# Kernel tuning notes

Measured on AMD Instinct MI355X. Metric: run time of the kernel, lower is better.

## Reference

```python
import jax, jax.numpy as jnp
import numpy as np

N, E = 20000, 160000
D_IN, HID, HEADS = 256, 64, 10
NEG_SLOPE = 0.2


def setup_inputs() -> dict:
    key = jax.random.key(0)
    ks = jax.random.split(key, 12)
    s = 0.05
    f = jnp.float32
    return {
        "x": jax.random.normal(ks[0], (N, D_IN), f),
        "edge_index": jax.random.randint(ks[1], (2, E), 0, N, jnp.int32),
        # GATConv 1: in=D_IN, out=HID, heads=10, concat=True
        "W1": (jax.random.normal(ks[2], (D_IN, HEADS * HID), f) * s),
        "a_src1": (jax.random.normal(ks[3], (HEADS, HID), f) * s),
        "a_dst1": (jax.random.normal(ks[4], (HEADS, HID), f) * s),
        "b1": jnp.zeros((HEADS * HID,), f),
        # GATConv 2: in=HEADS*HID, out=HID, heads=1
        "W2": (jax.random.normal(ks[5], (HEADS * HID, HID), f) * s),
        "a_src2": (jax.random.normal(ks[6], (1, HID), f) * s),
        "a_dst2": (jax.random.normal(ks[7], (1, HID), f) * s),
        "b2": jnp.zeros((HID,), f),
        # final Linear(hidden_dim, hidden_dim)
        "Wfc": (jax.random.normal(ks[8], (HID, HID), f) * s),
        "bfc": jnp.zeros((HID,), f),
    }


def gat_conv(x, src, dst, n, W, a_src, a_dst, b, heads, concat):
    """PyG GATConv (eval mode): gather, leaky-relu scores, segment softmax, scatter."""
    c = W.shape[1] // heads
    h = (x @ W).reshape(n, heads, c)                      # [N, H, C]
    score_src = jnp.sum(h * a_src, axis=-1)               # [N, H]
    score_dst = jnp.sum(h * a_dst, axis=-1)               # [N, H]
    e = jax.nn.leaky_relu(score_src[src] + score_dst[dst], NEG_SLOPE)  # [E, H]
    # segment softmax over incoming edges of each dst node
    m = jax.ops.segment_max(e, dst, num_segments=n)
    e = jnp.exp(e - m[dst])
    denom = jax.ops.segment_sum(e, dst, num_segments=n)
    alpha = e / (denom[dst] + 1e-16)                      # [E, H]
    msg = alpha[:, :, None] * h[src]                      # [E, H, C]
    out = jax.ops.segment_sum(msg, dst, num_segments=n)   # [N, H, C]
    out = out.reshape(n, heads * c) if concat else out.mean(axis=1)
    return out + b


def reference(x, edge_index, W1, a_src1, a_dst1, b1, W2, a_src2, a_dst2, b2, Wfc, bfc):
    n = x.shape[0]
    # add self loops (PyG default)
    loops = jnp.arange(n, dtype=edge_index.dtype)
    src = jnp.concatenate([edge_index[0], loops])
    dst = jnp.concatenate([edge_index[1], loops])
    h = jax.nn.relu(gat_conv(x, src, dst, n, W1, a_src1, a_dst1, b1, HEADS, True))
    h = jax.nn.relu(gat_conv(h, src, dst, n, W2, a_src2, a_dst2, b2, 1, True))
    return jax.nn.relu(h @ Wfc + bfc)
```

## Files before the change

kernel.cpp:

```cpp
#include <hip/hip_runtime.h>
#include <cstdint>
#include <cstddef>

constexpr int N_NODES = 20000;
constexpr int E_EDGES = 160000;
constexpr int D_INC   = 256;
constexpr int HEADSC  = 10;
constexpr int EN      = E_EDGES + N_NODES;
constexpr int ELLW    = 96;
constexpr float NEG_SLOPE = 0.2f;

typedef _Float16 half8 __attribute__((ext_vector_type(8)));
typedef float f32x4 __attribute__((ext_vector_type(4)));

__global__ __launch_bounds__(256) void gemm1_k(
    const float* __restrict__ X,
    const _Float16* __restrict__ BT,
    _Float16* __restrict__ C,
    const float* __restrict__ asv, const float* __restrict__ adv,
    float* __restrict__ s_s, float* __restrict__ s_d, int M)
{
    __shared__ alignas(16) _Float16 Ah[64][72];
    __shared__ alignas(16) _Float16 Bh[128][72];
    const int tid = threadIdx.x;
    const int wv  = tid >> 6;
    const int ln  = tid & 63;
    const int row0 = blockIdx.y * 64;
    const int col0 = blockIdx.x * 128;
    const int m = ln & 15;
    const int q = ln >> 4;
    const int arow = tid >> 2;
    const int acg  = (tid & 3) * 16;
    const int brow = tid >> 1;
    const int bcg  = (tid & 1) * 32;

    const bool aok = (row0 + arow) < M;
    const float*    xrow = X  + (size_t)(row0 + arow) * 256 + acg;
    const _Float16* bptr = BT + (size_t)(col0 + brow) * 256 + bcg;

    float4 av0, av1, av2, av3;
    int4   bv0, bv1, bv2, bv3;
    av0 = av1 = av2 = av3 = make_float4(0.f, 0.f, 0.f, 0.f);
    if (aok) {
        av0 = *reinterpret_cast<const float4*>(xrow);
        av1 = *reinterpret_cast<const float4*>(xrow + 4);
        av2 = *reinterpret_cast<const float4*>(xrow + 8);
        av3 = *reinterpret_cast<const float4*>(xrow + 12);
    }
    bv0 = *reinterpret_cast<const int4*>(bptr);
    bv1 = *reinterpret_cast<const int4*>(bptr + 8);
    bv2 = *reinterpret_cast<const int4*>(bptr + 16);
    bv3 = *reinterpret_cast<const int4*>(bptr + 24);

    f32x4 acc[8] = {};

    for (int k0 = 0; k0 < 256; k0 += 64) {
        half8 h0 = {(_Float16)av0.x, (_Float16)av0.y, (_Float16)av0.z, (_Float16)av0.w,
                    (_Float16)av1.x, (_Float16)av1.y, (_Float16)av1.z, (_Float16)av1.w};
        half8 h1v = {(_Float16)av2.x, (_Float16)av2.y, (_Float16)av2.z, (_Float16)av2.w,
                     (_Float16)av3.x, (_Float16)av3.y, (_Float16)av3.z, (_Float16)av3.w};
        *reinterpret_cast<half8*>(&Ah[arow][acg])     = h0;
        *reinterpret_cast<half8*>(&Ah[arow][acg + 8]) = h1v;
        *reinterpret_cast<int4*>(&Bh[brow][bcg])      = bv0;
        *reinterpret_cast<int4*>(&Bh[brow][bcg + 8])  = bv1;
        *reinterpret_cast<int4*>(&Bh[brow][bcg + 16]) = bv2;
        *reinterpret_cast<int4*>(&Bh[brow][bcg + 24]) = bv3;
        __syncthreads();

        if (k0 + 64 < 256) {
            const float* xp = xrow + k0 + 64;
            if (aok) {
                av0 = *reinterpret_cast<const float4*>(xp);
                av1 = *reinterpret_cast<const float4*>(xp + 4);
                av2 = *reinterpret_cast<const float4*>(xp + 8);
                av3 = *reinterpret_cast<const float4*>(xp + 12);
            }
            const _Float16* bp = bptr + k0 + 64;
            bv0 = *reinterpret_cast<const int4*>(bp);
            bv1 = *reinterpret_cast<const int4*>(bp + 8);
            bv2 = *reinterpret_cast<const int4*>(bp + 16);
            bv3 = *reinterpret_cast<const int4*>(bp + 24);
        }

#pragma unroll
        for (int ks = 0; ks < 2; ++ks) {
            const half8 af = *reinterpret_cast<const half8*>(
                &Ah[wv * 16 + m][ks * 32 + q * 8]);
#pragma unroll
            for (int ct = 0; ct < 8; ++ct) {
                const half8 bf = *reinterpret_cast<const half8*>(
                    &Bh[ct * 16 + m][ks * 32 + q * 8]);
                acc[ct] = __builtin_amdgcn_mfma_f32_16x16x32_f16(af, bf, acc[ct],
                                                                 0, 0, 0);
            }
        }
        __syncthreads();
    }

#pragma unroll
    for (int ct = 0; ct < 8; ++ct) {
#pragma unroll
        for (int r = 0; r < 4; ++r) {
            const int row = row0 + wv * 16 + q * 4 + r;
            if (row < M)
                C[(size_t)row * 640 + col0 + ct * 16 + m] = (_Float16)acc[ct][r];
        }
    }

    const int h0i = blockIdx.x * 2;
    float pa[2][4] = {}, pd[2][4] = {};
#pragma unroll
    for (int ct = 0; ct < 8; ++ct) {
        const int hh = ct >> 2;
        const int ch = (ct & 3) * 16 + m;
        const float a_ = asv[(h0i + hh) * 64 + ch];
        const float d_ = adv[(h0i + hh) * 64 + ch];
#pragma unroll
        for (int r = 0; r < 4; ++r) {
            pa[hh][r] += acc[ct][r] * a_;
            pd[hh][r] += acc[ct][r] * d_;
        }
    }
#pragma unroll
    for (int o = 1; o < 16; o <<= 1) {
#pragma unroll
        for (int hh = 0; hh < 2; ++hh)
#pragma unroll
            for (int r = 0; r < 4; ++r) {
                pa[hh][r] += __shfl_xor(pa[hh][r], o, 64);
                pd[hh][r] += __shfl_xor(pd[hh][r], o, 64);
            }
    }
    if (m == 0) {
#pragma unroll
        for (int hh = 0; hh < 2; ++hh)
#pragma unroll
            for (int r = 0; r < 4; ++r) {
                const int row = row0 + wv * 16 + q * 4 + r;
                if (row < M) {
                    s_s[row * HEADSC + h0i + hh] = pa[hh][r];
                    s_d[row * HEADSC + h0i + hh] = pd[hh][r];
                }
            }
    }
}

__global__ __launch_bounds__(128) void gemm2_k(
    const _Float16* __restrict__ A,
    const _Float16* __restrict__ BT,
    _Float16* __restrict__ C,
    const float* __restrict__ asv, const float* __restrict__ adv,
    float* __restrict__ s_s, float* __restrict__ s_d)
{
    __shared__ alignas(16) _Float16 Ah[32][72];
    __shared__ alignas(16) _Float16 Bh[64][72];
    const int tid = threadIdx.x;
    const int wv  = tid >> 6;
    const int ln  = tid & 63;
    const int row0 = blockIdx.x * 32;
    const int m = ln & 15;
    const int q = ln >> 4;
    const int arow = tid >> 2;
    const int acg  = (tid & 3) * 16;
    const int brow = tid >> 1;
    const int bcg  = (tid & 1) * 32;

    const _Float16* aptr = A  + (size_t)(row0 + arow) * 640 + acg;
    const _Float16* bptr = BT + (size_t)brow * 640 + bcg;

    int4 a0, a1, b0, b1, b2, b3;
    a0 = *reinterpret_cast<const int4*>(aptr);
    a1 = *reinterpret_cast<const int4*>(aptr + 8);
    b0 = *reinterpret_cast<const int4*>(bptr);
    b1 = *reinterpret_cast<const int4*>(bptr + 8);
    b2 = *reinterpret_cast<const int4*>(bptr + 16);
    b3 = *reinterpret_cast<const int4*>(bptr + 24);

    f32x4 acc[4] = {};

    for (int k0 = 0; k0 < 640; k0 += 64) {
        *reinterpret_cast<int4*>(&Ah[arow][acg])      = a0;
        *reinterpret_cast<int4*>(&Ah[arow][acg + 8])  = a1;
        *reinterpret_cast<int4*>(&Bh[brow][bcg])      = b0;
        *reinterpret_cast<int4*>(&Bh[brow][bcg + 8])  = b1;
        *reinterpret_cast<int4*>(&Bh[brow][bcg + 16]) = b2;
        *reinterpret_cast<int4*>(&Bh[brow][bcg + 24]) = b3;
        __syncthreads();

        if (k0 + 64 < 640) {
            const _Float16* ap = aptr + k0 + 64;
            a0 = *reinterpret_cast<const int4*>(ap);
            a1 = *reinterpret_cast<const int4*>(ap + 8);
            const _Float16* bp = bptr + k0 + 64;
            b0 = *reinterpret_cast<const int4*>(bp);
            b1 = *reinterpret_cast<const int4*>(bp + 8);
            b2 = *reinterpret_cast<const int4*>(bp + 16);
            b3 = *reinterpret_cast<const int4*>(bp + 24);
        }

#pragma unroll
        for (int ks = 0; ks < 2; ++ks) {
            const half8 af = *reinterpret_cast<const half8*>(
                &Ah[wv * 16 + m][ks * 32 + q * 8]);
#pragma unroll
            for (int ct = 0; ct < 4; ++ct) {
                const half8 bf = *reinterpret_cast<const half8*>(
                    &Bh[ct * 16 + m][ks * 32 + q * 8]);
                acc[ct] = __builtin_amdgcn_mfma_f32_16x16x32_f16(af, bf, acc[ct],
                                                                 0, 0, 0);
            }
        }
        __syncthreads();
    }

#pragma unroll
    for (int ct = 0; ct < 4; ++ct) {
#pragma unroll
        for (int r = 0; r < 4; ++r) {
            const int row = row0 + wv * 16 + q * 4 + r;
            C[(size_t)row * 64 + ct * 16 + m] = (_Float16)acc[ct][r];
        }
    }

    float pa[4] = {}, pd[4] = {};
#pragma unroll
    for (int ct = 0; ct < 4; ++ct) {
        const float a_ = asv[ct * 16 + m];
        const float d_ = adv[ct * 16 + m];
#pragma unroll
        for (int r = 0; r < 4; ++r) {
            pa[r] += acc[ct][r] * a_;
            pd[r] += acc[ct][r] * d_;
        }
    }
#pragma unroll
    for (int o = 1; o < 16; o <<= 1) {
#pragma unroll
        for (int r = 0; r < 4; ++r) {
            pa[r] += __shfl_xor(pa[r], o, 64);
            pd[r] += __shfl_xor(pd[r], o, 64);
        }
    }
    if (m == 0) {
#pragma unroll
        for (int r = 0; r < 4; ++r) {
            const int row = row0 + wv * 16 + q * 4 + r;
            s_s[row] = pa[r];
            s_d[row] = pd[r];
        }
    }
}

constexpr int W1E  = D_INC * 640;
constexpr int W2E  = 640 * 64;
constexpr int WFCE = 64 * 64;
constexpr int SETUP_TOT = EN + W1E + W2E + WFCE;

__global__ void setup_k(const int* __restrict__ src, const int* __restrict__ dst,
                        int* __restrict__ deg, int* __restrict__ ell,
                        const float* __restrict__ W1, const float* __restrict__ W2,
                        const float* __restrict__ Wfc,
                        _Float16* __restrict__ W1T, _Float16* __restrict__ W2T,
                        _Float16* __restrict__ WfcT)
{
    const int i = blockIdx.x * 256 + threadIdx.x;
    if (i < EN) {
        const int base = deg[N_NODES];
        int d, s;
        if (i < E_EDGES) { d = dst[i]; s = src[i]; }
        else             { d = i - E_EDGES; s = d; }
        const int r = atomicAdd(&deg[d], 1) - base;
        if ((unsigned)r < (unsigned)ELLW) ell[(size_t)d * ELLW + r] = s;
    } else if (i < EN + W1E) {
        const int j = i - EN;
        const int k = j / 640, n = j - k * 640;
        W1T[(size_t)n * D_INC + k] = (_Float16)W1[j];
    } else if (i < EN + W1E + W2E) {
        const int j = i - EN - W1E;
        const int k = j / 64, n = j - k * 64;
        W2T[(size_t)n * 640 + k] = (_Float16)W2[j];
    } else if (i < SETUP_TOT) {
        const int j = i - EN - W1E - W2E;
        const int k = j >> 6, n = j & 63;
        WfcT[(size_t)n * 64 + k] = (_Float16)Wfc[j];
    }
}

__global__ __launch_bounds__(320) void agg_f16_oct(
    const _Float16* __restrict__ h, const float* __restrict__ s_s,
    const float* __restrict__ s_d, const int* __restrict__ deg,
    const int* __restrict__ ell, const float* __restrict__ bias,
    _Float16* __restrict__ outp, int n_base)
{
    const int t   = blockIdx.x * 320 + threadIdx.x;
    const int n   = n_base + t / 80;
    const int oct = t - (t / 80) * 80;
    if (n >= N_NODES) return;
    const int hh  = oct >> 3;
    const _Float16* __restrict__ hb = h + oct * 8;
    const int* __restrict__ row = ell + (size_t)n * ELLW;
    const float sd = s_d[n * HEADSC + hh];
    const int dbase = deg[N_NODES];
    const int dc = min(deg[n] - dbase, ELLW);

    float acc[8] = {};
    float den = 0.f;
    int i = 0;
    for (; i + 3 < dc; i += 4) {
        const int s0 = row[i], s1 = row[i + 1], s2 = row[i + 2], s3 = row[i + 3];
        const float g0 = s_s[s0 * HEADSC + hh], g1 = s_s[s1 * HEADSC + hh];
        const float g2 = s_s[s2 * HEADSC + hh], g3 = s_s[s3 * HEADSC + hh];
        const half8 v0 = *reinterpret_cast<const half8*>(hb + (size_t)s0 * 640);
        const half8 v1 = *reinterpret_cast<const half8*>(hb + (size_t)s1 * 640);
        const half8 v2 = *reinterpret_cast<const half8*>(hb + (size_t)s2 * 640);
        const half8 v3 = *reinterpret_cast<const half8*>(hb + (size_t)s3 * 640);
        float e0 = g0 + sd, e1 = g1 + sd, e2 = g2 + sd, e3 = g3 + sd;
        e0 = (e0 > 0.f) ? e0 : NEG_SLOPE * e0;
        e1 = (e1 > 0.f) ? e1 : NEG_SLOPE * e1;
        e2 = (e2 > 0.f) ? e2 : NEG_SLOPE * e2;
        e3 = (e3 > 0.f) ? e3 : NEG_SLOPE * e3;
        const float w0 = __expf(e0), w1 = __expf(e1);
        const float w2 = __expf(e2), w3 = __expf(e3);
        den += (w0 + w1) + (w2 + w3);
#pragma unroll
        for (int j = 0; j < 8; ++j)
            acc[j] += (w0 * (float)v0[j] + w1 * (float)v1[j])
                    + (w2 * (float)v2[j] + w3 * (float)v3[j]);
    }
    for (; i < dc; ++i) {
        const int s0 = row[i];
        const float g0 = s_s[s0 * HEADSC + hh];
        const half8 v0 = *reinterpret_cast<const half8*>(hb + (size_t)s0 * 640);
        float e0 = g0 + sd;
        e0 = (e0 > 0.f) ? e0 : NEG_SLOPE * e0;
        const float w0 = __expf(e0);
        den += w0;
#pragma unroll
        for (int j = 0; j < 8; ++j) acc[j] += w0 * (float)v0[j];
    }
    const float inv = 1.f / (den + 1e-16f);
    const float* bb = bias + oct * 8;
    half8 o;
#pragma unroll
    for (int j = 0; j < 8; ++j)
        o[j] = (_Float16)fmaxf(acc[j] * inv + bb[j], 0.f);
    *reinterpret_cast<half8*>(outp + (size_t)n * 640 + oct * 8) = o;
}

__global__ __launch_bounds__(256) void agg2fc_k(
    const _Float16* __restrict__ h,
    const float* __restrict__ s_s, const float* __restrict__ s_d,
    const int* __restrict__ deg, const int* __restrict__ ell,
    const float* __restrict__ b2,
    const _Float16* __restrict__ WfcT,
    const float* __restrict__ bfc,
    float* __restrict__ out)
{
    __shared__ alignas(16) _Float16 Os[32][72];
    const int tid = threadIdx.x;
    const int n0  = blockIdx.x * 32;
    const int nl  = tid >> 3;
    const int oct = tid & 7;
    const int n   = n0 + nl;

    {
        const _Float16* __restrict__ hb = h + oct * 8;
        const int* __restrict__ row = ell + (size_t)n * ELLW;
        const float sd = s_d[n];
        const int dbase = deg[N_NODES];
        const int dc = min(deg[n] - dbase, ELLW);

        float acc[8] = {};
        float den = 0.f;
        int i = 0;
        for (; i + 3 < dc; i += 4) {
            int   sv[4];
            float gv[4];
            half8 hv[4];
#pragma unroll
            for (int u = 0; u < 4; ++u) sv[u] = row[i + u];
#pragma unroll
            for (int u = 0; u < 4; ++u) gv[u] = s_s[sv[u]];
#pragma unroll
            for (int u = 0; u < 4; ++u)
                hv[u] = *reinterpret_cast<const half8*>(hb + (size_t)sv[u] * 64);
#pragma unroll
            for (int u = 0; u < 4; ++u) {
                float e = gv[u] + sd;
                e = (e > 0.f) ? e : NEG_SLOPE * e;
                const float w = __expf(e);
                den += w;
#pragma unroll
                for (int j = 0; j < 8; ++j) acc[j] += w * (float)hv[u][j];
            }
        }
        for (; i < dc; ++i) {
            const int s0 = row[i];
            const float g0 = s_s[s0];
            const half8 v0 = *reinterpret_cast<const half8*>(hb + (size_t)s0 * 64);
            float e0 = g0 + sd;
            e0 = (e0 > 0.f) ? e0 : NEG_SLOPE * e0;
            const float w0 = __expf(e0);
            den += w0;
#pragma unroll
            for (int j = 0; j < 8; ++j) acc[j] += w0 * (float)v0[j];
        }
        const float inv = 1.f / (den + 1e-16f);
        const float* bb = b2 + oct * 8;
        half8 o;
#pragma unroll
        for (int j = 0; j < 8; ++j)
            o[j] = (_Float16)fmaxf(acc[j] * inv + bb[j], 0.f);
        *reinterpret_cast<half8*>(&Os[nl][oct * 8]) = o;
    }
    __syncthreads();

    const int wv = tid >> 6;
    const int ln = tid & 63;
    if (wv < 2) {
        const int m = ln & 15;
        const int q = ln >> 4;
        f32x4 acc[4] = {};
#pragma unroll
        for (int ks = 0; ks < 2; ++ks) {
            const half8 af = *reinterpret_cast<const half8*>(
                &Os[wv * 16 + m][ks * 32 + q * 8]);
#pragma unroll
            for (int ct = 0; ct < 4; ++ct) {
                const half8 bf = *reinterpret_cast<const half8*>(
                    WfcT + (size_t)(ct * 16 + m) * 64 + ks * 32 + q * 8);
                acc[ct] = __builtin_amdgcn_mfma_f32_16x16x32_f16(af, bf, acc[ct],
                                                                 0, 0, 0);
            }
        }
#pragma unroll
        for (int ct = 0; ct < 4; ++ct) {
#pragma unroll
            for (int r = 0; r < 4; ++r) {
                const int row = n0 + wv * 16 + q * 4 + r;
                const int col = ct * 16 + m;
                out[(size_t)row * 64 + col] = fmaxf(acc[ct][r] + bfc[col], 0.f);
            }
        }
    }
}

extern "C" void kernel_launch(void* const* d_in, const int* in_sizes, int n_in,
                              void* d_out, int out_size, void* d_ws, size_t ws_size,
                              hipStream_t stream)
{
    const float* x      = (const float*)d_in[0];
    const int*   edges  = (const int*)d_in[1];
    const float* W1     = (const float*)d_in[2];
    const float* a_src1 = (const float*)d_in[3];
    const float* a_dst1 = (const float*)d_in[4];
    const float* b1     = (const float*)d_in[5];
    const float* W2     = (const float*)d_in[6];
    const float* a_src2 = (const float*)d_in[7];
    const float* a_dst2 = (const float*)d_in[8];
    const float* b2     = (const float*)d_in[9];
    const float* Wfc    = (const float*)d_in[10];
    const float* bfc    = (const float*)d_in[11];
    float* out = (float*)d_out;

    const int* src = edges;
    const int* dst = edges + E_EDGES;

    char* ws = (char*)d_ws;
    size_t off = 0;
    auto alloc = [&](size_t bytes) -> void* {
        void* p = ws + off;
        off += (bytes + 255) & ~(size_t)255;
        return p;
    };
    _Float16*  h1     = (_Float16*)alloc((size_t)N_NODES * 640 * sizeof(_Float16));
    _Float16*  out1   = (_Float16*)alloc((size_t)N_NODES * 640 * sizeof(_Float16));
    _Float16*  h2     = (_Float16*)alloc((size_t)N_NODES * 64 * sizeof(_Float16));
    _Float16*  W1T    = (_Float16*)alloc((size_t)640 * D_INC * sizeof(_Float16));
    _Float16*  W2T    = (_Float16*)alloc((size_t)64 * 640 * sizeof(_Float16));
    _Float16*  WfcT   = (_Float16*)alloc((size_t)64 * 64 * sizeof(_Float16));
    float*     s_src1 = (float*)alloc((size_t)N_NODES * HEADSC * sizeof(float));
    float*     s_dst1 = (float*)alloc((size_t)N_NODES * HEADSC * sizeof(float));
    float*     s_src2 = (float*)alloc((size_t)N_NODES * sizeof(float));
    float*     s_dst2 = (float*)alloc((size_t)N_NODES * sizeof(float));
    int*       deg    = (int*)alloc((size_t)(N_NODES + 1) * sizeof(int));
    int*       ell    = (int*)alloc((size_t)N_NODES * ELLW * sizeof(int));

    setup_k<<<(SETUP_TOT + 255) / 256, 256, 0, stream>>>(
        src, dst, deg, ell, W1, W2, Wfc, W1T, W2T, WfcT);

    dim3 g1(5, (N_NODES + 63) / 64);
    gemm1_k<<<g1, 256, 0, stream>>>(x, W1T, h1, a_src1, a_dst1,
                                    s_src1, s_dst1, N_NODES);

    agg_f16_oct<<<2500, 320, 0, stream>>>(h1, s_src1, s_dst1, deg, ell, b1,
                                          out1, 0);
    agg_f16_oct<<<2500, 320, 0, stream>>>(h1, s_src1, s_dst1, deg, ell, b1,
                                          out1, 10000);

    gemm2_k<<<N_NODES / 32, 128, 0, stream>>>(out1, W2T, h2, a_src2, a_dst2,
                                              s_src2, s_dst2);

    agg2fc_k<<<N_NODES / 32, 256, 0, stream>>>(h2, s_src2, s_dst2, deg, ell,
                                               b2, WfcT, bfc, out);
}
```

Before: 187.4 us.

## Fuse all GAT stages into one persistent kernel with grid barriers

Replaces the six separate launches (setup, gemm1, two aggregation passes, gemm2, agg+fc) with one persistent kernel of 768 blocks. Stages are separated by software grid barriers built on global atomic counters, and the first GEMM hands out tiles through an atomic work counter. The aim is to remove per-launch overhead and inter-kernel gaps. In exchange it relies on all blocks being co-resident for the spin barriers, and the barrier waits and tile-counter atomics add synchronisation cost.

```diff
diff --git a/kernel.cpp b/kernel.cpp
--- a/kernel.cpp
+++ b/kernel.cpp
@@ -10,394 +10,242 @@
 constexpr int ELLW    = 96;
 constexpr float NEG_SLOPE = 0.2f;
 
-typedef _Float16 half8 __attribute__((ext_vector_type(8)));
-typedef float f32x4 __attribute__((ext_vector_type(4)));
-
-__global__ __launch_bounds__(256) void gemm1_k(
-    const float* __restrict__ X,
-    const _Float16* __restrict__ BT,
-    _Float16* __restrict__ C,
-    const float* __restrict__ asv, const float* __restrict__ adv,
-    float* __restrict__ s_s, float* __restrict__ s_d, int M)
-{
-    __shared__ alignas(16) _Float16 Ah[64][72];
-    __shared__ alignas(16) _Float16 Bh[128][72];
-    const int tid = threadIdx.x;
-    const int wv  = tid >> 6;
-    const int ln  = tid & 63;
-    const int row0 = blockIdx.y * 64;
-    const int col0 = blockIdx.x * 128;
-    const int m = ln & 15;
-    const int q = ln >> 4;
-    const int arow = tid >> 2;
-    const int acg  = (tid & 3) * 16;
-    const int brow = tid >> 1;
-    const int bcg  = (tid & 1) * 32;
-
-    const bool aok = (row0 + arow) < M;
-    const float*    xrow = X  + (size_t)(row0 + arow) * 256 + acg;
-    const _Float16* bptr = BT + (size_t)(col0 + brow) * 256 + bcg;
-
-    float4 av0, av1, av2, av3;
-    int4   bv0, bv1, bv2, bv3;
-    av0 = av1 = av2 = av3 = make_float4(0.f, 0.f, 0.f, 0.f);
-    if (aok) {
-        av0 = *reinterpret_cast<const float4*>(xrow);
-        av1 = *reinterpret_cast<const float4*>(xrow + 4);
-        av2 = *reinterpret_cast<const float4*>(xrow + 8);
-        av3 = *reinterpret_cast<const float4*>(xrow + 12);
-    }
-    bv0 = *reinterpret_cast<const int4*>(bptr);
-    bv1 = *reinterpret_cast<const int4*>(bptr + 8);
-    bv2 = *reinterpret_cast<const int4*>(bptr + 16);
-    bv3 = *reinterpret_cast<const int4*>(bptr + 24);
-
-    f32x4 acc[8] = {};
-
-    for (int k0 = 0; k0 < 256; k0 += 64) {
-        half8 h0 = {(_Float16)av0.x, (_Float16)av0.y, (_Float16)av0.z, (_Float16)av0.w,
-                    (_Float16)av1.x, (_Float16)av1.y, (_Float16)av1.z, (_Float16)av1.w};
-        half8 h1v = {(_Float16)av2.x, (_Float16)av2.y, (_Float16)av2.z, (_Float16)av2.w,
-                     (_Float16)av3.x, (_Float16)av3.y, (_Float16)av3.z, (_Float16)av3.w};
-        *reinterpret_cast<half8*>(&Ah[arow][acg])     = h0;
-        *reinterpret_cast<half8*>(&Ah[arow][acg + 8]) = h1v;
-        *reinterpret_cast<int4*>(&Bh[brow][bcg])      = bv0;
-        *reinterpret_cast<int4*>(&Bh[brow][bcg + 8])  = bv1;
-        *reinterpret_cast<int4*>(&Bh[brow][bcg + 16]) = bv2;
-        *reinterpret_cast<int4*>(&Bh[brow][bcg + 24]) = bv3;
-        __syncthreads();
-
-        if (k0 + 64 < 256) {
-            const float* xp = xrow + k0 + 64;
-            if (aok) {
-                av0 = *reinterpret_cast<const float4*>(xp);
-                av1 = *reinterpret_cast<const float4*>(xp + 4);
-                av2 = *reinterpret_cast<const float4*>(xp + 8);
-                av3 = *reinterpret_cast<const float4*>(xp + 12);
-            }
-            const _Float16* bp = bptr + k0 + 64;
-            bv0 = *reinterpret_cast<const int4*>(bp);
-            bv1 = *reinterpret_cast<const int4*>(bp + 8);
-            bv2 = *reinterpret_cast<const int4*>(bp + 16);
-            bv3 = *reinterpret_cast<const int4*>(bp + 24);
-        }
-
-#pragma unroll
-        for (int ks = 0; ks < 2; ++ks) {
-            const half8 af = *reinterpret_cast<const half8*>(
-                &Ah[wv * 16 + m][ks * 32 + q * 8]);
-#pragma unroll
-            for (int ct = 0; ct < 8; ++ct) {
-                const half8 bf = *reinterpret_cast<const half8*>(
-                    &Bh[ct * 16 + m][ks * 32 + q * 8]);
-                acc[ct] = __builtin_amdgcn_mfma_f32_16x16x32_f16(af, bf, acc[ct],
-                                                                 0, 0, 0);
-            }
-        }
-        __syncthreads();
-    }
-
-#pragma unroll
-    for (int ct = 0; ct < 8; ++ct) {
-#pragma unroll
-        for (int r = 0; r < 4; ++r) {
-            const int row = row0 + wv * 16 + q * 4 + r;
-            if (row < M)
-                C[(size_t)row * 640 + col0 + ct * 16 + m] = (_Float16)acc[ct][r];
-        }
-    }
-
-    const int h0i = blockIdx.x * 2;
-    float pa[2][4] = {}, pd[2][4] = {};
-#pragma unroll
-    for (int ct = 0; ct < 8; ++ct) {
-        const int hh = ct >> 2;
-        const int ch = (ct & 3) * 16 + m;
-        const float a_ = asv[(h0i + hh) * 64 + ch];
-        const float d_ = adv[(h0i + hh) * 64 + ch];
-#pragma unroll
-        for (int r = 0; r < 4; ++r) {
-            pa[hh][r] += acc[ct][r] * a_;
-            pd[hh][r] += acc[ct][r] * d_;
-        }
-    }
-#pragma unroll
-    for (int o = 1; o < 16; o <<= 1) {
-#pragma unroll
-        for (int hh = 0; hh < 2; ++hh)
-#pragma unroll
-            for (int r = 0; r < 4; ++r) {
-                pa[hh][r] += __shfl_xor(pa[hh][r], o, 64);
-                pd[hh][r] += __shfl_xor(pd[hh][r], o, 64);
-            }
-    }
-    if (m == 0) {
-#pragma unroll
-        for (int hh = 0; hh < 2; ++hh)
-#pragma unroll
-            for (int r = 0; r < 4; ++r) {
-                const int row = row0 + wv * 16 + q * 4 + r;
-                if (row < M) {
-                    s_s[row * HEADSC + h0i + hh] = pa[hh][r];
-                    s_d[row * HEADSC + h0i + hh] = pd[hh][r];
-                }
-            }
-    }
-}
-
-__global__ __launch_bounds__(128) void gemm2_k(
-    const _Float16* __restrict__ A,
-    const _Float16* __restrict__ BT,
-    _Float16* __restrict__ C,
-    const float* __restrict__ asv, const float* __restrict__ adv,
-    float* __restrict__ s_s, float* __restrict__ s_d)
-{
-    __shared__ alignas(16) _Float16 Ah[32][72];
-    __shared__ alignas(16) _Float16 Bh[64][72];
-    const int tid = threadIdx.x;
-    const int wv  = tid >> 6;
-    const int ln  = tid & 63;
-    const int row0 = blockIdx.x * 32;
-    const int m = ln & 15;
-    const int q = ln >> 4;
-    const int arow = tid >> 2;
-    const int acg  = (tid & 3) * 16;
-    const int brow = tid >> 1;
-    const int bcg  = (tid & 1) * 32;
-
-    const _Float16* aptr = A  + (size_t)(row0 + arow) * 640 + acg;
-    const _Float16* bptr = BT + (size_t)brow * 640 + bcg;
-
-    int4 a0, a1, b0, b1, b2, b3;
-    a0 = *reinterpret_cast<const int4*>(aptr);
-    a1 = *reinterpret_cast<const int4*>(aptr + 8);
-    b0 = *reinterpret_cast<const int4*>(bptr);
-    b1 = *reinterpret_cast<const int4*>(bptr + 8);
-    b2 = *reinterpret_cast<const int4*>(bptr + 16);
-    b3 = *reinterpret_cast<const int4*>(bptr + 24);
-
-    f32x4 acc[4] = {};
-
-    for (int k0 = 0; k0 < 640; k0 += 64) {
-        *reinterpret_cast<int4*>(&Ah[arow][acg])      = a0;
-        *reinterpret_cast<int4*>(&Ah[arow][acg + 8])  = a1;
-        *reinterpret_cast<int4*>(&Bh[brow][bcg])      = b0;
-        *reinterpret_cast<int4*>(&Bh[brow][bcg + 8])  = b1;
-        *reinterpret_cast<int4*>(&Bh[brow][bcg + 16]) = b2;
-        *reinterpret_cast<int4*>(&Bh[brow][bcg + 24]) = b3;
-        __syncthreads();
-
-        if (k0 + 64 < 640) {
-            const _Float16* ap = aptr + k0 + 64;
-            a0 = *reinterpret_cast<const int4*>(ap);
-            a1 = *reinterpret_cast<const int4*>(ap + 8);
-            const _Float16* bp = bptr + k0 + 64;
-            b0 = *reinterpret_cast<const int4*>(bp);
-            b1 = *reinterpret_cast<const int4*>(bp + 8);
-            b2 = *reinterpret_cast<const int4*>(bp + 16);
-            b3 = *reinterpret_cast<const int4*>(bp + 24);
-        }
-
-#pragma unroll
-        for (int ks = 0; ks < 2; ++ks) {
-            const half8 af = *reinterpret_cast<const half8*>(
-                &Ah[wv * 16 + m][ks * 32 + q * 8]);
-#pragma unroll
-            for (int ct = 0; ct < 4; ++ct) {
-                const half8 bf = *reinterpret_cast<const half8*>(
-                    &Bh[ct * 16 + m][ks * 32 + q * 8]);
-                acc[ct] = __builtin_amdgcn_mfma_f32_16x16x32_f16(af, bf, acc[ct],
-                                                                 0, 0, 0);
-            }
-        }
-        __syncthreads();
-    }
-
-#pragma unroll
-    for (int ct = 0; ct < 4; ++ct) {
-#pragma unroll
-        for (int r = 0; r < 4; ++r) {
-            const int row = row0 + wv * 16 + q * 4 + r;
-            C[(size_t)row * 64 + ct * 16 + m] = (_Float16)acc[ct][r];
-        }
-    }
-
-    float pa[4] = {}, pd[4] = {};
-#pragma unroll
-    for (int ct = 0; ct < 4; ++ct) {
-        const float a_ = asv[ct * 16 + m];
-        const float d_ = adv[ct * 16 + m];
-#pragma unroll
-        for (int r = 0; r < 4; ++r) {
-            pa[r] += acc[ct][r] * a_;
-            pd[r] += acc[ct][r] * d_;
-        }
-    }
-#pragma unroll
-    for (int o = 1; o < 16; o <<= 1) {
-#pragma unroll
-        for (int r = 0; r < 4; ++r) {
-            pa[r] += __shfl_xor(pa[r], o, 64);
-            pd[r] += __shfl_xor(pd[r], o, 64);
-        }
-    }
-    if (m == 0) {
-#pragma unroll
-        for (int r = 0; r < 4; ++r) {
-            const int row = row0 + wv * 16 + q * 4 + r;
-            s_s[row] = pa[r];
-            s_d[row] = pd[r];
-        }
-    }
-}
+constexpr int NBLK = 768;
+constexpr int BSZ  = 256;
+constexpr int GSZ  = NBLK * BSZ;
 
 constexpr int W1E  = D_INC * 640;
 constexpr int W2E  = 640 * 64;
 constexpr int WFCE = 64 * 64;
 constexpr int SETUP_TOT = EN + W1E + W2E + WFCE;
-
-__global__ void setup_k(const int* __restrict__ src, const int* __restrict__ dst,
-                        int* __restrict__ deg, int* __restrict__ ell,
-                        const float* __restrict__ W1, const float* __restrict__ W2,
-                        const float* __restrict__ Wfc,
-                        _Float16* __restrict__ W1T, _Float16* __restrict__ W2T,
-                        _Float16* __restrict__ WfcT)
+constexpr int NT1 = 5 * 313;
+
+typedef _Float16 half8 __attribute__((ext_vector_type(8)));
+typedef float f32x4 __attribute__((ext_vector_type(4)));
+
+__device__ __forceinline__ void gbar(unsigned* bars, int i, unsigned base)
 {
-    const int i = blockIdx.x * 256 + threadIdx.x;
-    if (i < EN) {
-        const int base = deg[N_NODES];
-        int d, s;
-        if (i < E_EDGES) { d = dst[i]; s = src[i]; }
-        else             { d = i - E_EDGES; s = d; }
-        const int r = atomicAdd(&deg[d], 1) - base;
-        if ((unsigned)r < (unsigned)ELLW) ell[(size_t)d * ELLW + r] = s;
-    } else if (i < EN + W1E) {
-        const int j = i - EN;
-        const int k = j / 640, n = j - k * 640;
-        W1T[(size_t)n * D_INC + k] = (_Float16)W1[j];
-    } else if (i < EN + W1E + W2E) {
-        const int j = i - EN - W1E;
-        const int k = j / 64, n = j - k * 64;
-        W2T[(size_t)n * 640 + k] = (_Float16)W2[j];
-    } else if (i < SETUP_TOT) {
-        const int j = i - EN - W1E - W2E;
-        const int k = j >> 6, n = j & 63;
-        WfcT[(size_t)n * 64 + k] = (_Float16)Wfc[j];
-    }
+    __syncthreads();
+    if (threadIdx.x == 0) {
+        __threadfence();
+        __hip_atomic_fetch_add(&bars[i], 1u, __ATOMIC_RELEASE,
+                               __HIP_MEMORY_SCOPE_AGENT);
+        while (__hip_atomic_load(&bars[i], __ATOMIC_ACQUIRE,
+                                 __HIP_MEMORY_SCOPE_AGENT) - base < (unsigned)NBLK)
+            __builtin_amdgcn_s_sleep(2);
+        __threadfence();
+    }
+    __syncthreads();
 }
 
-__global__ __launch_bounds__(320) void agg_f16_oct(
-    const _Float16* __restrict__ h, const float* __restrict__ s_s,
-    const float* __restrict__ s_d, const int* __restrict__ deg,
-    const int* __restrict__ ell, const float* __restrict__ bias,
-    _Float16* __restrict__ outp, int n_base)
+__global__ __launch_bounds__(BSZ, 4) void mega_k(
+    const float* __restrict__ X, const int* __restrict__ esrc,
+    const int* __restrict__ edst,
+    const float* __restrict__ W1, const float* __restrict__ as1,
+    const float* __restrict__ ad1, const float* __restrict__ b1,
+    const float* __restrict__ W2, const float* __restrict__ as2,
+    const float* __restrict__ ad2, const float* __restrict__ b2,
+    const float* __restrict__ Wfc, const float* __restrict__ bfc,
+    float* __restrict__ out,
+    _Float16* __restrict__ h1, _Float16* __restrict__ out1,
+    _Float16* __restrict__ h2,
+    _Float16* __restrict__ W1T, _Float16* __restrict__ W2T,
+    _Float16* __restrict__ WfcT,
+    float* __restrict__ ss1, float* __restrict__ sd1,
+    float* __restrict__ ss2, float* __restrict__ sd2,
+    int* __restrict__ deg, int* __restrict__ ell,
+    unsigned* __restrict__ bars)
 {
-    const int t   = blockIdx.x * 320 + threadIdx.x;
-    const int n   = n_base + t / 80;
-    const int oct = t - (t / 80) * 80;
-    if (n >= N_NODES) return;
-    const int hh  = oct >> 3;
-    const _Float16* __restrict__ hb = h + oct * 8;
-    const int* __restrict__ row = ell + (size_t)n * ELLW;
-    const float sd = s_d[n * HEADSC + hh];
+    __shared__ alignas(16) char SMEM[27648];
+    __shared__ int tile_s;
+    const int tid  = threadIdx.x;
+    const int bid  = blockIdx.x;
+    const int gtid = bid * BSZ + tid;
+    const unsigned base = bars[63];
     const int dbase = deg[N_NODES];
-    const int dc = min(deg[n] - dbase, ELLW);
-
-    float acc[8] = {};
-    float den = 0.f;
-    int i = 0;
-    for (; i + 3 < dc; i += 4) {
-        const int s0 = row[i], s1 = row[i + 1], s2 = row[i + 2], s3 = row[i + 3];
-        const float g0 = s_s[s0 * HEADSC + hh], g1 = s_s[s1 * HEADSC + hh];
-        const float g2 = s_s[s2 * HEADSC + hh], g3 = s_s[s3 * HEADSC + hh];
-        const half8 v0 = *reinterpret_cast<const half8*>(hb + (size_t)s0 * 640);
-        const half8 v1 = *reinterpret_cast<const half8*>(hb + (size_t)s1 * 640);
-        const half8 v2 = *reinterpret_cast<const half8*>(hb + (size_t)s2 * 640);
-        const half8 v3 = *reinterpret_cast<const half8*>(hb + (size_t)s3 * 640);
-        float e0 = g0 + sd, e1 = g1 + sd, e2 = g2 + sd, e3 = g3 + sd;
-        e0 = (e0 > 0.f) ? e0 : NEG_SLOPE * e0;
-        e1 = (e1 > 0.f) ? e1 : NEG_SLOPE * e1;
-        e2 = (e2 > 0.f) ? e2 : NEG_SLOPE * e2;
-        e3 = (e3 > 0.f) ? e3 : NEG_SLOPE * e3;
-        const float w0 = __expf(e0), w1 = __expf(e1);
-        const float w2 = __expf(e2), w3 = __expf(e3);
-        den += (w0 + w1) + (w2 + w3);
-#pragma unroll
-        for (int j = 0; j < 8; ++j)
-            acc[j] += (w0 * (float)v0[j] + w1 * (float)v1[j])
-                    + (w2 * (float)v2[j] + w3 * (float)v3[j]);
-    }
-    for (; i < dc; ++i) {
-        const int s0 = row[i];
-        const float g0 = s_s[s0 * HEADSC + hh];
-        const half8 v0 = *reinterpret_cast<const half8*>(hb + (size_t)s0 * 640);
-        float e0 = g0 + sd;
-        e0 = (e0 > 0.f) ? e0 : NEG_SLOPE * e0;
-        const float w0 = __expf(e0);
-        den += w0;
-#pragma unroll
-        for (int j = 0; j < 8; ++j) acc[j] += w0 * (float)v0[j];
-    }
-    const float inv = 1.f / (den + 1e-16f);
-    const float* bb = bias + oct * 8;
-    half8 o;
-#pragma unroll
-    for (int j = 0; j < 8; ++j)
-        o[j] = (_Float16)fmaxf(acc[j] * inv + bb[j], 0.f);
-    *reinterpret_cast<half8*>(outp + (size_t)n * 640 + oct * 8) = o;
-}
-
-__global__ __launch_bounds__(256) void agg2fc_k(
-    const _Float16* __restrict__ h,
-    const float* __restrict__ s_s, const float* __restrict__ s_d,
-    const int* __restrict__ deg, const int* __restrict__ ell,
-    const float* __restrict__ b2,
-    const _Float16* __restrict__ WfcT,
-    const float* __restrict__ bfc,
-    float* __restrict__ out)
-{
-    __shared__ alignas(16) _Float16 Os[32][72];
-    const int tid = threadIdx.x;
-    const int n0  = blockIdx.x * 32;
-    const int nl  = tid >> 3;
-    const int oct = tid & 7;
-    const int n   = n0 + nl;
+
+    for (int i = gtid; i < SETUP_TOT; i += GSZ) {
+        if (i < EN) {
+            int d, s;
+            if (i < E_EDGES) { d = edst[i]; s = esrc[i]; }
+            else             { d = i - E_EDGES; s = d; }
+            const int r = atomicAdd(&deg[d], 1) - dbase;
+            if ((unsigned)r < (unsigned)ELLW) ell[(size_t)d * ELLW + r] = s;
+        } else if (i < EN + W1E) {
+            const int j = i - EN;
+            const int k = j / 640, n = j - k * 640;
+            W1T[(size_t)n * D_INC + k] = (_Float16)W1[j];
+        } else if (i < EN + W1E + W2E) {
+            const int j = i - EN - W1E;
+            const int k = j / 64, n = j - k * 64;
+            W2T[(size_t)n * 640 + k] = (_Float16)W2[j];
+        } else {
+            const int j = i - EN - W1E - W2E;
+            const int k = j >> 6, n = j & 63;
+            WfcT[(size_t)n * 64 + k] = (_Float16)Wfc[j];
+        }
+    }
+    gbar(bars, 0, base);
 
     {
-        const _Float16* __restrict__ hb = h + oct * 8;
+        auto Ah = reinterpret_cast<_Float16(*)[72]>(SMEM);
+        auto Bh = reinterpret_cast<_Float16(*)[72]>(SMEM + 9216);
+        const int wv = tid >> 6, ln = tid & 63;
+        const int m = ln & 15, q = ln >> 4;
+        const int arow = tid >> 2, acg = (tid & 3) * 16;
+        const int brow = tid >> 1, bcg = (tid & 1) * 32;
+        for (;;) {
+            __syncthreads();
+            if (tid == 0)
+                tile_s = (int)(__hip_atomic_fetch_add(&bars[32], 1u,
+                               __ATOMIC_RELAXED, __HIP_MEMORY_SCOPE_AGENT) - base);
+            __syncthreads();
+            const int t = tile_s;
+            if (t >= NT1) break;
+            const int by = t / 5, bx = t - by * 5;
+            const int row0 = by * 64, col0 = bx * 128;
+            const int ar_c = min(row0 + arow, N_NODES - 1);
+            const float*    xrow = X   + (size_t)ar_c * 256 + acg;
+            const _Float16* bptr = W1T + (size_t)(col0 + brow) * 256 + bcg;
+
+            float4 av0 = *reinterpret_cast<const float4*>(xrow);
+            float4 av1 = *reinterpret_cast<const float4*>(xrow + 4);
+            float4 av2 = *reinterpret_cast<const float4*>(xrow + 8);
+            float4 av3 = *reinterpret_cast<const float4*>(xrow + 12);
+            int4   bv0 = *reinterpret_cast<const int4*>(bptr);
+            int4   bv1 = *reinterpret_cast<const int4*>(bptr + 8);
+            int4   bv2 = *reinterpret_cast<const int4*>(bptr + 16);
+            int4   bv3 = *reinterpret_cast<const int4*>(bptr + 24);
+
+            f32x4 acc[8] = {};
+            for (int k0 = 0; k0 < 256; k0 += 64) {
+                half8 ha0 = {(_Float16)av0.x, (_Float16)av0.y, (_Float16)av0.z,
+                             (_Float16)av0.w, (_Float16)av1.x, (_Float16)av1.y,
+                             (_Float16)av1.z, (_Float16)av1.w};
+                half8 ha1 = {(_Float16)av2.x, (_Float16)av2.y, (_Float16)av2.z,
+                             (_Float16)av2.w, (_Float16)av3.x, (_Float16)av3.y,
+                             (_Float16)av3.z, (_Float16)av3.w};
+                *reinterpret_cast<half8*>(&Ah[arow][acg])     = ha0;
+                *reinterpret_cast<half8*>(&Ah[arow][acg + 8]) = ha1;
+                *reinterpret_cast<int4*>(&Bh[brow][bcg])      = bv0;
+                *reinterpret_cast<int4*>(&Bh[brow][bcg + 8])  = bv1;
+                *reinterpret_cast<int4*>(&Bh[brow][bcg + 16]) = bv2;
+                *reinterpret_cast<int4*>(&Bh[brow][bcg + 24]) = bv3;
+                __syncthreads();
+                if (k0 + 64 < 256) {
+                    const float* xp = xrow + k0 + 64;
+                    av0 = *reinterpret_cast<const float4*>(xp);
+                    av1 = *reinterpret_cast<const float4*>(xp + 4);
+                    av2 = *reinterpret_cast<const float4*>(xp + 8);
+                    av3 = *reinterpret_cast<const float4*>(xp + 12);
+                    const _Float16* bp = bptr + k0 + 64;
+                    bv0 = *reinterpret_cast<const int4*>(bp);
+                    bv1 = *reinterpret_cast<const int4*>(bp + 8);
+                    bv2 = *reinterpret_cast<const int4*>(bp + 16);
+                    bv3 = *reinterpret_cast<const int4*>(bp + 24);
+                }
+#pragma unroll
+                for (int ks = 0; ks < 2; ++ks) {
+                    const half8 af = *reinterpret_cast<const half8*>(
+                        &Ah[wv * 16 + m][ks * 32 + q * 8]);
+#pragma unroll
+                    for (int ct = 0; ct < 8; ++ct) {
+                        const half8 bf = *reinterpret_cast<const half8*>(
+                            &Bh[ct * 16 + m][ks * 32 + q * 8]);
+                        acc[ct] = __builtin_amdgcn_mfma_f32_16x16x32_f16(
+                            af, bf, acc[ct], 0, 0, 0);
+                    }
+                }
+                __syncthreads();
+            }
+
+#pragma unroll
+            for (int ct = 0; ct < 8; ++ct) {
+#pragma unroll
+                for (int r = 0; r < 4; ++r) {
+                    const int row = row0 + wv * 16 + q * 4 + r;
+                    if (row < N_NODES)
+                        h1[(size_t)row * 640 + col0 + ct * 16 + m] =
+                            (_Float16)acc[ct][r];
+                }
+            }
+            const int h0i = bx * 2;
+            float pa[2][4] = {}, pd[2][4] = {};
+#pragma unroll
+            for (int ct = 0; ct < 8; ++ct) {
+                const int hh = ct >> 2;
+                const int ch = (ct & 3) * 16 + m;
+                const float a_ = as1[(h0i + hh) * 64 + ch];
+                const float d_ = ad1[(h0i + hh) * 64 + ch];
+#pragma unroll
+                for (int r = 0; r < 4; ++r) {
+                    pa[hh][r] += acc[ct][r] * a_;
+                    pd[hh][r] += acc[ct][r] * d_;
+                }
+            }
+#pragma unroll
+            for (int o = 1; o < 16; o <<= 1) {
+#pragma unroll
+                for (int hh = 0; hh < 2; ++hh)
+#pragma unroll
+                    for (int r = 0; r < 4; ++r) {
+                        pa[hh][r] += __shfl_xor(pa[hh][r], o, 64);
+                        pd[hh][r] += __shfl_xor(pd[hh][r], o, 64);
+                    }
+            }
+            if (m == 0) {
+#pragma unroll
+                for (int hh = 0; hh < 2; ++hh)
+#pragma unroll
+                    for (int r = 0; r < 4; ++r) {
+                        const int row = row0 + wv * 16 + q * 4 + r;
+                        if (row < N_NODES) {
+                            ss1[row * HEADSC + h0i + hh] = pa[hh][r];
+                            sd1[row * HEADSC + h0i + hh] = pd[hh][r];
+                        }
+                    }
+            }
+        }
+    }
+    gbar(bars, 1, base);
+
+    for (int idx = gtid; idx < N_NODES * 80; idx += GSZ) {
+        const int n   = idx / 80;
+        const int oct = idx - n * 80;
+        const int hh  = oct >> 3;
+        const _Float16* __restrict__ hb = h1 + oct * 8;
         const int* __restrict__ row = ell + (size_t)n * ELLW;
-        const float sd = s_d[n];
-        const int dbase = deg[N_NODES];
+        const float sd = sd1[n * HEADSC + hh];
         const int dc = min(deg[n] - dbase, ELLW);
 
         float acc[8] = {};
         float den = 0.f;
         int i = 0;
         for (; i + 3 < dc; i += 4) {
-            int   sv[4];
-            float gv[4];
-            half8 hv[4];
-#pragma unroll
-            for (int u = 0; u < 4; ++u) sv[u] = row[i + u];
-#pragma unroll
-            for (int u = 0; u < 4; ++u) gv[u] = s_s[sv[u]];
-#pragma unroll
-            for (int u = 0; u < 4; ++u)
-                hv[u] = *reinterpret_cast<const half8*>(hb + (size_t)sv[u] * 64);
-#pragma unroll
-            for (int u = 0; u < 4; ++u) {
-                float e = gv[u] + sd;
-                e = (e > 0.f) ? e : NEG_SLOPE * e;
-                const float w = __expf(e);
-                den += w;
-#pragma unroll
-                for (int j = 0; j < 8; ++j) acc[j] += w * (float)hv[u][j];
-            }
+            const int s0 = row[i], s1 = row[i + 1], s2 = row[i + 2], s3 = row[i + 3];
+            const float g0 = ss1[s0 * HEADSC + hh], g1 = ss1[s1 * HEADSC + hh];
+            const float g2 = ss1[s2 * HEADSC + hh], g3 = ss1[s3 * HEADSC + hh];
+            const half8 v0 = *reinterpret_cast<const half8*>(hb + (size_t)s0 * 640);
+            const half8 v1 = *reinterpret_cast<const half8*>(hb + (size_t)s1 * 640);
+            const half8 v2 = *reinterpret_cast<const half8*>(hb + (size_t)s2 * 640);
+            const half8 v3 = *reinterpret_cast<const half8*>(hb + (size_t)s3 * 640);
+            float e0 = g0 + sd, e1 = g1 + sd, e2 = g2 + sd, e3 = g3 + sd;
+            e0 = (e0 > 0.f) ? e0 : NEG_SLOPE * e0;
+            e1 = (e1 > 0.f) ? e1 : NEG_SLOPE * e1;
+            e2 = (e2 > 0.f) ? e2 : NEG_SLOPE * e2;
+            e3 = (e3 > 0.f) ? e3 : NEG_SLOPE * e3;
+            const float w0 = __expf(e0), w1 = __expf(e1);
+            const float w2 = __expf(e2), w3 = __expf(e3);
+            den += (w0 + w1) + (w2 + w3);
+#pragma unroll
+            for (int j = 0; j < 8; ++j)
+                acc[j] += (w0 * (float)v0[j] + w1 * (float)v1[j])
+                        + (w2 * (float)v2[j] + w3 * (float)v3[j]);
         }
         for (; i < dc; ++i) {
             const int s0 = row[i];
-            const float g0 = s_s[s0];
-            const half8 v0 = *reinterpret_cast<const half8*>(hb + (size_t)s0 * 64);
+            const float g0 = ss1[s0 * HEADSC + hh];
+            const half8 v0 = *reinterpret_cast<const half8*>(hb + (size_t)s0 * 640);
             float e0 = g0 + sd;
             e0 = (e0 > 0.f) ? e0 : NEG_SLOPE * e0;
             const float w0 = __expf(e0);
@@ -406,40 +254,181 @@
             for (int j = 0; j < 8; ++j) acc[j] += w0 * (float)v0[j];
         }
         const float inv = 1.f / (den + 1e-16f);
-        const float* bb = b2 + oct * 8;
+        const float* bb = b1 + oct * 8;
         half8 o;
 #pragma unroll
         for (int j = 0; j < 8; ++j)
             o[j] = (_Float16)fmaxf(acc[j] * inv + bb[j], 0.f);
-        *reinterpret_cast<half8*>(&Os[nl][oct * 8]) = o;
-    }
-    __syncthreads();
-
-    const int wv = tid >> 6;
-    const int ln = tid & 63;
-    if (wv < 2) {
-        const int m = ln & 15;
-        const int q = ln >> 4;
+        *reinterpret_cast<half8*>(out1 + (size_t)n * 640 + oct * 8) = o;
+    }
+    gbar(bars, 2, base);
+
+    if (bid < 313) {
+        auto Ah = reinterpret_cast<_Float16(*)[72]>(SMEM);
+        auto Bh = reinterpret_cast<_Float16(*)[72]>(SMEM + 9216);
+        const int wv = tid >> 6, ln = tid & 63;
+        const int m = ln & 15, q = ln >> 4;
+        const int arow = tid >> 2, acg = (tid & 3) * 16;
+        const int row0 = bid * 64;
+        const int ar_c = min(row0 + arow, N_NODES - 1);
+        const _Float16* aptr = out1 + (size_t)ar_c * 640 + acg;
+        const _Float16* bptr = W2T + (size_t)arow * 640 + acg;
+
+        int4 a0 = *reinterpret_cast<const int4*>(aptr);
+        int4 a1 = *reinterpret_cast<const int4*>(aptr + 8);
+        int4 b0 = *reinterpret_cast<const int4*>(bptr);
+        int4 b1 = *reinterpret_cast<const int4*>(bptr + 8);
+
         f32x4 acc[4] = {};
-#pragma unroll
-        for (int ks = 0; ks < 2; ++ks) {
-            const half8 af = *reinterpret_cast<const half8*>(
-                &Os[wv * 16 + m][ks * 32 + q * 8]);
+        for (int k0 = 0; k0 < 640; k0 += 64) {
+            *reinterpret_cast<int4*>(&Ah[arow][acg])     = a0;
+            *reinterpret_cast<int4*>(&Ah[arow][acg + 8]) = a1;
+            *reinterpret_cast<int4*>(&Bh[arow][acg])     = b0;
+            *reinterpret_cast<int4*>(&Bh[arow][acg + 8]) = b1;
+            __syncthreads();
+            if (k0 + 64 < 640) {
+                a0 = *reinterpret_cast<const int4*>(aptr + k0 + 64);
+                a1 = *reinterpret_cast<const int4*>(aptr + k0 + 72);
+                b0 = *reinterpret_cast<const int4*>(bptr + k0 + 64);
+                b1 = *reinterpret_cast<const int4*>(bptr + k0 + 72);
+            }
+#pragma unroll
+            for (int ks = 0; ks < 2; ++ks) {
+                const half8 af = *reinterpret_cast<const half8*>(
+                    &Ah[wv * 16 + m][ks * 32 + q * 8]);
+#pragma unroll
+                for (int ct = 0; ct < 4; ++ct) {
+                    const half8 bf = *reinterpret_cast<const half8*>(
+                        &Bh[ct * 16 + m][ks * 32 + q * 8]);
+                    acc[ct] = __builtin_amdgcn_mfma_f32_16x16x32_f16(
+                        af, bf, acc[ct], 0, 0, 0);
+                }
+            }
+            __syncthreads();
+        }
+
+#pragma unroll
+        for (int ct = 0; ct < 4; ++ct) {
+#pragma unroll
+            for (int r = 0; r < 4; ++r) {
+                const int row = row0 + wv * 16 + q * 4 + r;
+                if (row < N_NODES)
+                    h2[(size_t)row * 64 + ct * 16 + m] = (_Float16)acc[ct][r];
+            }
+        }
+        float pa[4] = {}, pd[4] = {};
+#pragma unroll
+        for (int ct = 0; ct < 4; ++ct) {
+            const float a_ = as2[ct * 16 + m];
+            const float d_ = ad2[ct * 16 + m];
+#pragma unroll
+            for (int r = 0; r < 4; ++r) {
+                pa[r] += acc[ct][r] * a_;
+                pd[r] += acc[ct][r] * d_;
+            }
+        }
+#pragma unroll
+        for (int o = 1; o < 16; o <<= 1) {
+#pragma unroll
+            for (int r = 0; r < 4; ++r) {
+                pa[r] += __shfl_xor(pa[r], o, 64);
+                pd[r] += __shfl_xor(pd[r], o, 64);
+            }
+        }
+        if (m == 0) {
+#pragma unroll
+            for (int r = 0; r < 4; ++r) {
+                const int row = row0 + wv * 16 + q * 4 + r;
+                if (row < N_NODES) { ss2[row] = pa[r]; sd2[row] = pd[r]; }
+            }
+        }
+    }
+    gbar(bars, 3, base);
+
+    if (bid < 625) {
+        auto Os = reinterpret_cast<_Float16(*)[72]>(SMEM);
+        const int n0  = bid * 32;
+        const int nl  = tid >> 3;
+        const int oct = tid & 7;
+        const int n   = n0 + nl;
+
+        {
+            const _Float16* __restrict__ hb = h2 + oct * 8;
+            const int* __restrict__ row = ell + (size_t)n * ELLW;
+            const float sd = sd2[n];
+            const int dc = min(deg[n] - dbase, ELLW);
+
+            float acc[8] = {};
+            float den = 0.f;
+            int i = 0;
+            for (; i + 3 < dc; i += 4) {
+                int   sv[4];
+                float gv[4];
+                half8 hv[4];
+#pragma unroll
+                for (int u = 0; u < 4; ++u) sv[u] = row[i + u];
+#pragma unroll
+                for (int u = 0; u < 4; ++u) gv[u] = ss2[sv[u]];
+#pragma unroll
+                for (int u = 0; u < 4; ++u)
+                    hv[u] = *reinterpret_cast<const half8*>(hb + (size_t)sv[u] * 64);
+#pragma unroll
+                for (int u = 0; u < 4; ++u) {
+                    float e = gv[u] + sd;
+                    e = (e > 0.f) ? e : NEG_SLOPE * e;
+                    const float w = __expf(e);
+                    den += w;
+#pragma unroll
+                    for (int j = 0; j < 8; ++j) acc[j] += w * (float)hv[u][j];
+                }
+            }
+            for (; i < dc; ++i) {
+                const int s0 = row[i];
+                const float g0 = ss2[s0];
+                const half8 v0 = *reinterpret_cast<const half8*>(hb + (size_t)s0 * 64);
+                float e0 = g0 + sd;
+                e0 = (e0 > 0.f) ? e0 : NEG_SLOPE * e0;
+                const float w0 = __expf(e0);
+                den += w0;
+#pragma unroll
+                for (int j = 0; j < 8; ++j) acc[j] += w0 * (float)v0[j];
+            }
+            const float inv = 1.f / (den + 1e-16f);
+            const float* bb = b2 + oct * 8;
+            half8 o;
+#pragma unroll
+            for (int j = 0; j < 8; ++j)
+                o[j] = (_Float16)fmaxf(acc[j] * inv + bb[j], 0.f);
+            *reinterpret_cast<half8*>(&Os[nl][oct * 8]) = o;
+        }
+        __syncthreads();
+
+        const int wv = tid >> 6;
+        const int ln = tid & 63;
+        if (wv < 2) {
+            const int m = ln & 15;
+            const int q = ln >> 4;
+            f32x4 acc[4] = {};
+#pragma unroll
+            for (int ks = 0; ks < 2; ++ks) {
+                const half8 af = *reinterpret_cast<const half8*>(
+                    &Os[wv * 16 + m][ks * 32 + q * 8]);
+#pragma unroll
+                for (int ct = 0; ct < 4; ++ct) {
+                    const half8 bf = *reinterpret_cast<const half8*>(
+                        WfcT + (size_t)(ct * 16 + m) * 64 + ks * 32 + q * 8);
+                    acc[ct] = __builtin_amdgcn_mfma_f32_16x16x32_f16(
+                        af, bf, acc[ct], 0, 0, 0);
+                }
+            }
 #pragma unroll
             for (int ct = 0; ct < 4; ++ct) {
-                const half8 bf = *reinterpret_cast<const half8*>(
-                    WfcT + (size_t)(ct * 16 + m) * 64 + ks * 32 + q * 8);
-                acc[ct] = __builtin_amdgcn_mfma_f32_16x16x32_f16(af, bf, acc[ct],
-                                                                 0, 0, 0);
-            }
-        }
-#pragma unroll
-        for (int ct = 0; ct < 4; ++ct) {
-#pragma unroll
-            for (int r = 0; r < 4; ++r) {
-                const int row = n0 + wv * 16 + q * 4 + r;
-                const int col = ct * 16 + m;
-                out[(size_t)row * 64 + col] = fmaxf(acc[ct][r] + bfc[col], 0.f);
+#pragma unroll
+                for (int r = 0; r < 4; ++r) {
+                    const int row = n0 + wv * 16 + q * 4 + r;
+                    const int col = ct * 16 + m;
+                    out[(size_t)row * 64 + col] = fmaxf(acc[ct][r] + bfc[col], 0.f);
+                }
             }
         }
     }
@@ -473,34 +462,25 @@
         off += (bytes + 255) & ~(size_t)255;
         return p;
     };
-    _Float16*  h1     = (_Float16*)alloc((size_t)N_NODES * 640 * sizeof(_Float16));
-    _Float16*  out1   = (_Float16*)alloc((size_t)N_NODES * 640 * sizeof(_Float16));
-    _Float16*  h2     = (_Float16*)alloc((size_t)N_NODES * 64 * sizeof(_Float16));
-    _Float16*  W1T    = (_Float16*)alloc((size_t)640 * D_INC * sizeof(_Float16));
-    _Float16*  W2T    = (_Float16*)alloc((size_t)64 * 640 * sizeof(_Float16));
-    _Float16*  WfcT   = (_Float16*)alloc((size_t)64 * 64 * sizeof(_Float16));
-    float*     s_src1 = (float*)alloc((size_t)N_NODES * HEADSC * sizeof(float));
-    float*     s_dst1 = (float*)alloc((size_t)N_NODES * HEADSC * sizeof(float));
-    float*     s_src2 = (float*)alloc((size_t)N_NODES * sizeof(float));
-    float*     s_dst2 = (float*)alloc((size_t)N_NODES * sizeof(float));
-    int*       deg    = (int*)alloc((size_t)(N_NODES + 1) * sizeof(int));
-    int*       ell    = (int*)alloc((size_t)N_NODES * ELLW * sizeof(int));
-
-    setup_k<<<(SETUP_TOT + 255) / 256, 256, 0, stream>>>(
-        src, dst, deg, ell, W1, W2, Wfc, W1T, W2T, WfcT);
-
-    dim3 g1(5, (N_NODES + 63) / 64);
-    gemm1_k<<<g1, 256, 0, stream>>>(x, W1T, h1, a_src1, a_dst1,
-                                    s_src1, s_dst1, N_NODES);
-
-    agg_f16_oct<<<2500, 320, 0, stream>>>(h1, s_src1, s_dst1, deg, ell, b1,
-                                          out1, 0);
-    agg_f16_oct<<<2500, 320, 0, stream>>>(h1, s_src1, s_dst1, deg, ell, b1,
-                                          out1, 10000);
-
-    gemm2_k<<<N_NODES / 32, 128, 0, stream>>>(out1, W2T, h2, a_src2, a_dst2,
-                                              s_src2, s_dst2);
-
-    agg2fc_k<<<N_NODES / 32, 256, 0, stream>>>(h2, s_src2, s_dst2, deg, ell,
-                                               b2, WfcT, bfc, out);
+    _Float16*  h1   = (_Float16*)alloc((size_t)N_NODES * 640 * sizeof(_Float16));
+    _Float16*  out1 = (_Float16*)alloc((size_t)N_NODES * 640 * sizeof(_Float16));
+    _Float16*  h2   = (_Float16*)alloc((size_t)N_NODES * 64 * sizeof(_Float16));
+    _Float16*  W1T  = (_Float16*)alloc((size_t)640 * D_INC * sizeof(_Float16));
+    _Float16*  W2T  = (_Float16*)alloc((size_t)64 * 640 * sizeof(_Float16));
+    _Float16*  WfcT = (_Float16*)alloc((size_t)64 * 64 * sizeof(_Float16));
+    float*     ss1  = (float*)alloc((size_t)N_NODES * HEADSC * sizeof(float));
+    float*     sd1  = (float*)alloc((size_t)N_NODES * HEADSC * sizeof(float));
+    float*     ss2  = (float*)alloc((size_t)N_NODES * sizeof(float));
+    float*     sd2  = (float*)alloc((size_t)N_NODES * sizeof(float));
+    int*       deg  = (int*)alloc((size_t)(N_NODES + 1) * sizeof(int));
+    int*       ell  = (int*)alloc((size_t)N_NODES * ELLW * sizeof(int));
+    unsigned*  bars = (unsigned*)alloc(256);
+
+    mega_k<<<NBLK, BSZ, 0, stream>>>(
+        x, src, dst,
+        W1, a_src1, a_dst1, b1,
+        W2, a_src2, a_dst2, b2,
+        Wfc, bfc, out,
+        h1, out1, h2, W1T, W2T, WfcT,
+        ss1, sd1, ss2, sd2, deg, ell, bars);
 }
```

New measurement: 747.8 us. 3.99x slower.
